# Kernel tuning notes

Measured on AMD Instinct MI355X. Metric: run time of the kernel, lower is better.

## Reference

```python
import jax, jax.numpy as jnp
import numpy as np
from jax import lax

T_LEN, BATCH, IN_DIM, HID = 1024, 64, 256, 256


def setup_inputs() -> dict:
    key = jax.random.key(0)
    k1, k2, k3, k4 = jax.random.split(key, 4)
    x = jax.random.normal(k1, (T_LEN, BATCH, IN_DIM), dtype=jnp.float32)
    m = jax.random.normal(k2, (T_LEN, BATCH, HID), dtype=jnp.float32)
    h0 = jnp.zeros((BATCH, HID), dtype=jnp.float32)
    c0 = jnp.zeros((BATCH, HID), dtype=jnp.float32)
    # 5 gates: input, forget, cell, output, reinstatement
    scale = 1.0 / np.sqrt(HID)
    W_ih = jax.random.normal(k3, (5 * HID, IN_DIM), dtype=jnp.float32) * scale
    W_hh = jax.random.normal(k4, (5 * HID, HID), dtype=jnp.float32) * scale
    b = jnp.zeros((5 * HID,), dtype=jnp.float32)
    return {"x": x, "m": m, "h0": h0, "c0": c0, "W_ih": W_ih, "W_hh": W_hh, "b": b}


def reference(x, m, h0, c0, W_ih, W_hh, b):
    """Episodic LSTM: sequential scan over time (batch_first=False, forward direction).

    x: [T, B, I], m: [T, B, H] (retrieved episodic cell states per step).
    Returns (sequence [T, B, H], h_T [B, H], c_T [B, H]).
    """
    # Precompute input projections for all timesteps in one GEMM: [T, B, 5H]
    x_proj = jnp.einsum("tbi,gi->tbg", x, W_ih) + b

    def step(carry, inp):
        h, c = carry
        xp_t, m_t = inp
        gates = xp_t + h @ W_hh.T  # [B, 5H]
        i, f, g, o, r = jnp.split(gates, 5, axis=-1)
        c = (jax.nn.sigmoid(f) * c
             + jax.nn.sigmoid(i) * jnp.tanh(g)
             + jax.nn.sigmoid(r) * m_t)
        h = jax.nn.sigmoid(o) * jnp.tanh(c)
        return (h, c), h

    (hT, cT), seq = lax.scan(step, (h0, c0), (x_proj, m))
    return seq, hT, cT
```

## Files before the change

kernel.cpp:

```cpp
#include <hip/hip_runtime.h>
#include <stdint.h>
#include <stddef.h>

#define T_LEN 1024
#define BATCH 64
#define KDIM  256
#define HID   256
#define NGATE 5
#define GROWS (NGATE * HID)
#define NGT   (GROWS / 16)
#define NSWG  4

typedef __attribute__((ext_vector_type(8))) short s16x8;
typedef __attribute__((ext_vector_type(4))) float f32x4;
typedef __attribute__((ext_vector_type(4))) int   i32x4;
typedef __attribute__((ext_vector_type(2))) unsigned int u32x2;

static __device__ __forceinline__ uint16_t f2bf(float f) {
  uint32_t u = __float_as_uint(f);
  return (uint16_t)((u + 0x7fffu + ((u >> 16) & 1u)) >> 16);
}
static __device__ __forceinline__ float bf2f(uint16_t b) {
  return __uint_as_float(((uint32_t)b) << 16);
}
static __device__ __forceinline__ s16x8 cvt8(const float* __restrict__ p) {
  float4 a = *reinterpret_cast<const float4*>(p);
  float4 b = *reinterpret_cast<const float4*>(p + 4);
  union { s16x8 v; uint16_t u[8]; } r;
  r.u[0] = f2bf(a.x); r.u[1] = f2bf(a.y); r.u[2] = f2bf(a.z); r.u[3] = f2bf(a.w);
  r.u[4] = f2bf(b.x); r.u[5] = f2bf(b.y); r.u[6] = f2bf(b.z); r.u[7] = f2bf(b.w);
  return r.v;
}
static __device__ __forceinline__ float sigm(float x)   { return 1.f / (1.f + __expf(-x)); }
static __device__ __forceinline__ float tanh_f(float x) { return 1.f - 2.f / (__expf(2.f * x) + 1.f); }
static __device__ __forceinline__ int swz(int row, int col) {
  return ((((col >> 4) ^ (row & 15)) << 4) | (col & 15));
}

__global__ void setup_kernel(const float* __restrict__ Wih, const float* __restrict__ c0,
                             uint16_t* __restrict__ wihb, float* __restrict__ cbuf) {
  int i = blockIdx.x * 256 + threadIdx.x;
  if (i < GROWS * KDIM) wihb[i] = f2bf(Wih[i]);
  if (i < BATCH * HID) cbuf[i] = c0[i];
}

__global__ void wquant_kernel(const float* __restrict__ Whh,
                              int8_t* __restrict__ wq, float* __restrict__ wsc) {
  int row = blockIdx.x * 256 + threadIdx.x;
  if (row >= GROWS) return;
  const float* wr = Whh + (size_t)row * KDIM;
  float mx = 1e-30f;
  for (int k = 0; k < KDIM; ++k) mx = fmaxf(mx, fabsf(wr[k]));
  wsc[row] = mx / 127.f;
  const float inv = 127.f / mx;
  int8_t* q = wq + (size_t)row * KDIM;
  for (int k = 0; k < KDIM; ++k) q[k] = (int8_t)__float2int_rn(wr[k] * inv);
}

__global__ __launch_bounds__(256, 2)
void xproj_kernel(const float* __restrict__ x, const uint16_t* __restrict__ wihb,
                  const float* __restrict__ bias, uint16_t* __restrict__ xp, int t0) {
  const int w = threadIdx.x >> 6, lane = threadIdx.x & 63;
  const int r16 = lane & 15, ke = (lane >> 4) * 8;
  const int tA = t0 + (int)blockIdx.x * 2;

  s16x8 A[2][8];
#pragma unroll
  for (int tt = 0; tt < 2; ++tt) {
    const float* ap = x + ((size_t)(tA + tt) * BATCH + w * 16 + r16) * KDIM + ke;
#pragma unroll
    for (int ks = 0; ks < 8; ++ks) A[tt][ks] = cvt8(ap + ks * 32);
  }
  for (int gt = 0; gt < NGT; ++gt) {
    const uint16_t* bp = wihb + (size_t)(gt * 16 + r16) * KDIM + ke;
    s16x8 B[8];
#pragma unroll
    for (int ks = 0; ks < 8; ++ks) B[ks] = *reinterpret_cast<const s16x8*>(bp + ks * 32);
    const float bv = bias[gt * 16 + r16];
#pragma unroll
    for (int tt = 0; tt < 2; ++tt) {
      f32x4 acc = {};
#pragma unroll
      for (int ks = 0; ks < 8; ++ks)
        acc = __builtin_amdgcn_mfma_f32_16x16x32_bf16(A[tt][ks], B[ks], acc, 0, 0, 0);
      const int lt = (int)blockIdx.x * 2 + tt;
      uint32_t w0 = (uint32_t)f2bf(acc[0] + bv) | ((uint32_t)f2bf(acc[1] + bv) << 16);
      uint32_t w1 = (uint32_t)f2bf(acc[2] + bv) | ((uint32_t)f2bf(acc[3] + bv) << 16);
      u32x2 pk = {w0, w1};
      u32x2* dst = (u32x2*)((uint32_t*)(xp + ((size_t)(lt * 4 + w) * NGT + gt) * 256) + lane * 2);
      __builtin_nontemporal_store(pk, dst);
    }
  }
}

__global__ __launch_bounds__(1024, 4)
void scan_kernel(const float* __restrict__ mIn, const int8_t* __restrict__ wq,
                 const float* __restrict__ wsc, const uint16_t* __restrict__ xp,
                 const float* __restrict__ h_src, float* __restrict__ cbuf,
                 float* __restrict__ seq, float* __restrict__ hT, float* __restrict__ cT,
                 int s0, int s1) {
  struct SW {
    int8_t w[16][2][4][1024];
    int8_t hq[2][16][256];
  };
  __shared__ SW sl;
  const int wg = blockIdx.x;
  const int v = threadIdx.x >> 6;
  const int lane = threadIdx.x & 63;
  const int r16 = lane & 15, g4 = lane >> 4;
  const int bj0 = g4 * 4;
  const int brow = wg * 16;
  const int col = v * 16 + r16;

  i32x4 Wf[3][4];
  float sc[NGATE];
#pragma unroll
  for (int g = 0; g < NGATE; ++g) {
    const int grow = g * 256 + col;
    if (g < 3) {
      const int8_t* wp = wq + (size_t)grow * KDIM + g4 * 16;
#pragma unroll
      for (int ks = 0; ks < 4; ++ks)
        Wf[g][ks] = *reinterpret_cast<const i32x4*>(wp + ks * 64);
    }
    sc[g] = wsc[grow] * (1.f / 127.f);
  }
#pragma unroll
  for (int gl = 0; gl < 2; ++gl) {
    const int grow = (3 + gl) * 256 + col;
    const int8_t* wp = wq + (size_t)grow * KDIM + g4 * 16;
#pragma unroll
    for (int ks = 0; ks < 4; ++ks)
      *reinterpret_cast<i32x4*>(&sl.w[v][gl][ks][lane * 16]) =
          *reinterpret_cast<const i32x4*>(wp + ks * 64);
  }

  float c[4];
#pragma unroll
  for (int j = 0; j < 4; ++j)
    c[j] = cbuf[(size_t)(brow + bj0 + j) * HID + col];

  {
    const int p0 = s0 & 1;
#pragma unroll
    for (int e = 0; e < 4; ++e) {
      int t = (int)threadIdx.x * 4 + e;
      int row = t >> 8, cc = t & 255;
      float hv = h_src[(size_t)(brow + row) * HID + cc];
      int q = __float2int_rn(fminf(fmaxf(hv * 127.f, -127.f), 127.f));
      sl.hq[p0][row][swz(row, cc)] = (int8_t)q;
    }
  }
  __syncthreads();

  const uint16_t* xpb = xp + ((size_t)wg * NGT + v) * 256 + lane * 4;
  const float*    mb  = mIn + ((size_t)s0 * BATCH + brow + bj0) * HID + col;
  float*          sqb = seq + ((size_t)s0 * BATCH + brow + bj0) * HID + col;

  u32x2 xpf[NGATE];
  float mv[4];
#pragma unroll
  for (int g = 0; g < NGATE; ++g)
    xpf[g] = *reinterpret_cast<const u32x2*>(xpb + g * 16 * 256);
#pragma unroll
  for (int j = 0; j < 4; ++j) mv[j] = mb[j * HID];

  for (int s = s0; s < s1; ++s) {
    const int p = s & 1;

    i32x4 acc[NGATE] = {};
    __builtin_amdgcn_s_setprio(1);
#pragma unroll
    for (int ks = 0; ks < 4; ++ks) {
      i32x4 A = *reinterpret_cast<const i32x4*>(&sl.hq[p][r16][swz(r16, (g4 + 4 * ks) * 16)]);
      acc[0] = __builtin_amdgcn_mfma_i32_16x16x64_i8(A, Wf[0][ks], acc[0], 0, 0, 0);
      acc[1] = __builtin_amdgcn_mfma_i32_16x16x64_i8(A, Wf[1][ks], acc[1], 0, 0, 0);
      acc[2] = __builtin_amdgcn_mfma_i32_16x16x64_i8(A, Wf[2][ks], acc[2], 0, 0, 0);
      i32x4 b0 = *reinterpret_cast<const i32x4*>(&sl.w[v][0][ks][lane * 16]);
      acc[3] = __builtin_amdgcn_mfma_i32_16x16x64_i8(A, b0, acc[3], 0, 0, 0);
      i32x4 b1 = *reinterpret_cast<const i32x4*>(&sl.w[v][1][ks][lane * 16]);
      acc[4] = __builtin_amdgcn_mfma_i32_16x16x64_i8(A, b1, acc[4], 0, 0, 0);
    }
    __builtin_amdgcn_s_setprio(0);

    float hnew[4];
#pragma unroll
    for (int j = 0; j < 4; ++j) {
#define XPV(g) bf2f((uint16_t)((j & 1) ? (xpf[g][j >> 1] >> 16) : (xpf[g][j >> 1] & 0xffff)))
      const float gi = (float)acc[0][j] * sc[0] + XPV(0);
      const float gf = (float)acc[1][j] * sc[1] + XPV(1);
      const float gg = (float)acc[2][j] * sc[2] + XPV(2);
      const float go = (float)acc[3][j] * sc[3] + XPV(3);
      const float gr = (float)acc[4][j] * sc[4] + XPV(4);
#undef XPV
      const float cn = sigm(gf) * c[j] + sigm(gi) * tanh_f(gg) + sigm(gr) * mv[j];
      c[j] = cn;
      hnew[j] = sigm(go) * tanh_f(cn);
    }

    const uint16_t* xpb_n = xpb + 4 * NGT * 256;
    const float*    mb_n  = (s + 1 < s1) ? mb + BATCH * HID : mb;
#pragma unroll
    for (int g = 0; g < NGATE; ++g)
      xpf[g] = *reinterpret_cast<const u32x2*>(xpb_n + g * 16 * 256);
#pragma unroll
    for (int j = 0; j < 4; ++j) mv[j] = mb_n[j * HID];
    xpb = xpb_n; mb = mb_n;

#pragma unroll
    for (int j = 0; j < 4; ++j) {
      __builtin_nontemporal_store(hnew[j], sqb + j * HID);
      int q = __float2int_rn(hnew[j] * 127.f);
      sl.hq[p ^ 1][bj0 + j][swz(bj0 + j, col)] = (int8_t)q;
    }
    if (s == T_LEN - 1) {
#pragma unroll
      for (int j = 0; j < 4; ++j) {
        hT[(size_t)(brow + bj0 + j) * HID + col] = hnew[j];
        cT[(size_t)(brow + bj0 + j) * HID + col] = c[j];
      }
    }
    sqb += BATCH * HID;

    __builtin_amdgcn_sched_barrier(0);
    asm volatile("s_waitcnt lgkmcnt(0)" ::: "memory");
    __builtin_amdgcn_s_barrier();
    __builtin_amdgcn_sched_barrier(0);
  }

#pragma unroll
  for (int j = 0; j < 4; ++j)
    cbuf[(size_t)(brow + bj0 + j) * HID + col] = c[j];
}

extern "C" void kernel_launch(void* const* d_in, const int* in_sizes, int n_in,
                              void* d_out, int out_size, void* d_ws, size_t ws_size,
                              hipStream_t stream) {
  (void)in_sizes; (void)n_in; (void)out_size;
  const float* x    = (const float*)d_in[0];
  const float* mIn  = (const float*)d_in[1];
  const float* h0   = (const float*)d_in[2];
  const float* c0   = (const float*)d_in[3];
  const float* Wih  = (const float*)d_in[4];
  const float* Whh  = (const float*)d_in[5];
  const float* bias = (const float*)d_in[6];
  float* out = (float*)d_out;
  float* seq = out;
  float* hT  = out + (size_t)T_LEN * BATCH * HID;
  float* cT  = hT + (size_t)BATCH * HID;

  const size_t fixed = (size_t)GROWS * KDIM * 2 + (size_t)GROWS * KDIM
                     + (size_t)GROWS * 4 + (size_t)BATCH * HID * 4 + 4096;
  int tchunk = T_LEN;
  while (tchunk > 2 && (size_t)tchunk * BATCH * GROWS * 2 + fixed > ws_size) tchunk >>= 1;

  char* p = (char*)d_ws;
  uint16_t* xp   = (uint16_t*)p;  p += (size_t)tchunk * BATCH * GROWS * 2;
  uint16_t* wihb = (uint16_t*)p;  p += (size_t)GROWS * KDIM * 2;
  int8_t*   wq   = (int8_t*)p;    p += (size_t)GROWS * KDIM;
  float*    wsc  = (float*)p;     p += (size_t)GROWS * 4;
  float*    cbuf = (float*)p;

  setup_kernel<<<dim3((GROWS * KDIM + 255) / 256), dim3(256), 0, stream>>>(
      Wih, c0, wihb, cbuf);
  wquant_kernel<<<dim3((GROWS + 255) / 256), dim3(256), 0, stream>>>(Whh, wq, wsc);
  for (int s0 = 0; s0 < T_LEN; s0 += tchunk) {
    xproj_kernel<<<dim3(tchunk / 2), dim3(256), 0, stream>>>(x, wihb, bias, xp, s0);
    const float* h_src = (s0 == 0) ? h0 : (seq + (size_t)(s0 - 1) * BATCH * HID);
    scan_kernel<<<dim3(NSWG), dim3(1024), 0, stream>>>(
        mIn, wq, wsc, xp, h_src, cbuf, seq, hT, cT, s0, s0 + tchunk);
  }
}
```

Measured before the change: 4.004 ms.

## Hold all recurrent weights in AGPRs, fold log2e into weights, unroll scan by two

All five int8 W_hh gate slices now stay in registers, fed to inline-asm MFMAs as AGPR operands, so the two gates that used LDS no longer reload it every step. log2(e) factors are folded into W_ih, the bias and the per-row scales so the activations can use raw v_exp_f32 and v_rcp_f32. The time loop is unrolled by two with separate prefetch buffers for xp and m, which removes the parity math. The trade-offs are higher register pressure and reliance on inline asm, which limits compiler scheduling. The loop also assumes s1-s0 is even and hard-codes parity 0 as the start, which could break for odd chunk boundaries.

Measured after the change: 6.730 ms. 68.1% more time.

```diff
diff --git a/kernel.cpp b/kernel.cpp
--- a/kernel.cpp
+++ b/kernel.cpp
@@ -11,6 +11,9 @@
 #define NGT   (GROWS / 16)
 #define NSWG  4
 
+#define L2E  1.442695041f
+#define L2E2 2.885390082f
+
 typedef __attribute__((ext_vector_type(8))) short s16x8;
 typedef __attribute__((ext_vector_type(4))) float f32x4;
 typedef __attribute__((ext_vector_type(4))) int   i32x4;
@@ -31,16 +34,38 @@
   r.u[4] = f2bf(b.x); r.u[5] = f2bf(b.y); r.u[6] = f2bf(b.z); r.u[7] = f2bf(b.w);
   return r.v;
 }
-static __device__ __forceinline__ float sigm(float x)   { return 1.f / (1.f + __expf(-x)); }
-static __device__ __forceinline__ float tanh_f(float x) { return 1.f - 2.f / (__expf(2.f * x) + 1.f); }
+static __device__ __forceinline__ float rcp_hw(float x) {
+  float r; asm("v_rcp_f32 %0, %1" : "=v"(r) : "v"(x)); return r;
+}
+static __device__ __forceinline__ float exp2_hw(float x) {
+  float r; asm("v_exp_f32 %0, %1" : "=v"(r) : "v"(x)); return r;
+}
+static __device__ __forceinline__ float exp2_neg(float x) {
+  float r; asm("v_exp_f32 %0, -%1" : "=v"(r) : "v"(x)); return r;
+}
+static __device__ __forceinline__ float sigm2(float xs) {
+  return rcp_hw(1.f + exp2_neg(xs));
+}
+static __device__ __forceinline__ float tanh2(float xs) {
+  return __builtin_fmaf(-2.f, rcp_hw(1.f + exp2_hw(xs)), 1.f);
+}
 static __device__ __forceinline__ int swz(int row, int col) {
   return ((((col >> 4) ^ (row & 15)) << 4) | (col & 15));
 }
+
+#define MFMA_A(acc, A, W) \
+  asm("v_mfma_i32_16x16x64_i8 %0, %1, %2, %0" : "+v"(acc) : "v"(A), "a"(W))
+#define MFMA_I(acc, A, W, Z) \
+  asm("v_mfma_i32_16x16x64_i8 %0, %1, %2, %3" : "=&v"(acc) : "v"(A), "a"(W), "v"(Z))
 
 __global__ void setup_kernel(const float* __restrict__ Wih, const float* __restrict__ c0,
                              uint16_t* __restrict__ wihb, float* __restrict__ cbuf) {
   int i = blockIdx.x * 256 + threadIdx.x;
-  if (i < GROWS * KDIM) wihb[i] = f2bf(Wih[i]);
+  if (i < GROWS * KDIM) {
+    int gate = (i >> 8) >> 8;
+    float kg = (gate == 2) ? L2E2 : L2E;
+    wihb[i] = f2bf(Wih[i] * kg);
+  }
   if (i < BATCH * HID) cbuf[i] = c0[i];
 }
 
@@ -76,7 +101,8 @@
     s16x8 B[8];
 #pragma unroll
     for (int ks = 0; ks < 8; ++ks) B[ks] = *reinterpret_cast<const s16x8*>(bp + ks * 32);
-    const float bv = bias[gt * 16 + r16];
+    const float kg = ((gt >> 4) == 2) ? L2E2 : L2E;
+    const float bv = bias[gt * 16 + r16] * kg;
 #pragma unroll
     for (int tt = 0; tt < 2; ++tt) {
       f32x4 acc = {};
@@ -99,11 +125,7 @@
                  const float* __restrict__ h_src, float* __restrict__ cbuf,
                  float* __restrict__ seq, float* __restrict__ hT, float* __restrict__ cT,
                  int s0, int s1) {
-  struct SW {
-    int8_t w[16][2][4][1024];
-    int8_t hq[2][16][256];
-  };
-  __shared__ SW sl;
+  __shared__ int8_t hq[2][16][256];
   const int wg = blockIdx.x;
   const int v = threadIdx.x >> 6;
   const int lane = threadIdx.x & 63;
@@ -112,27 +134,16 @@
   const int brow = wg * 16;
   const int col = v * 16 + r16;
 
-  i32x4 Wf[3][4];
+  i32x4 Wf[NGATE][4];
   float sc[NGATE];
 #pragma unroll
   for (int g = 0; g < NGATE; ++g) {
-    const int grow = g * 256 + col;
-    if (g < 3) {
-      const int8_t* wp = wq + (size_t)grow * KDIM + g4 * 16;
-#pragma unroll
-      for (int ks = 0; ks < 4; ++ks)
-        Wf[g][ks] = *reinterpret_cast<const i32x4*>(wp + ks * 64);
-    }
-    sc[g] = wsc[grow] * (1.f / 127.f);
-  }
-#pragma unroll
-  for (int gl = 0; gl < 2; ++gl) {
-    const int grow = (3 + gl) * 256 + col;
-    const int8_t* wp = wq + (size_t)grow * KDIM + g4 * 16;
+    const float kg = (g == 2) ? L2E2 : L2E;
+    sc[g] = wsc[g * 256 + col] * (kg / 127.f);
+    const int8_t* wp = wq + (size_t)(g * 256 + col) * KDIM + g4 * 16;
 #pragma unroll
     for (int ks = 0; ks < 4; ++ks)
-      *reinterpret_cast<i32x4*>(&sl.w[v][gl][ks][lane * 16]) =
-          *reinterpret_cast<const i32x4*>(wp + ks * 64);
+      Wf[g][ks] = *reinterpret_cast<const i32x4*>(wp + ks * 64);
   }
 
   float c[4];
@@ -140,46 +151,61 @@
   for (int j = 0; j < 4; ++j)
     c[j] = cbuf[(size_t)(brow + bj0 + j) * HID + col];
 
-  {
-    const int p0 = s0 & 1;
-#pragma unroll
-    for (int e = 0; e < 4; ++e) {
-      int t = (int)threadIdx.x * 4 + e;
-      int row = t >> 8, cc = t & 255;
-      float hv = h_src[(size_t)(brow + row) * HID + cc];
-      int q = __float2int_rn(fminf(fmaxf(hv * 127.f, -127.f), 127.f));
-      sl.hq[p0][row][swz(row, cc)] = (int8_t)q;
-    }
+#pragma unroll
+  for (int e = 0; e < 4; ++e) {
+    int t = (int)threadIdx.x * 4 + e;
+    int row = t >> 8, cc = t & 255;
+    float hv = h_src[(size_t)(brow + row) * HID + cc];
+    int q = __float2int_rn(fminf(fmaxf(hv * 127.f, -127.f), 127.f));
+    hq[0][row][swz(row, cc)] = (int8_t)q;
   }
   __syncthreads();
 
-  const uint16_t* xpb = xp + ((size_t)wg * NGT + v) * 256 + lane * 4;
-  const float*    mb  = mIn + ((size_t)s0 * BATCH + brow + bj0) * HID + col;
-  float*          sqb = seq + ((size_t)s0 * BATCH + brow + bj0) * HID + col;
-
-  u32x2 xpf[NGATE];
-  float mv[4];
-#pragma unroll
-  for (int g = 0; g < NGATE; ++g)
-    xpf[g] = *reinterpret_cast<const u32x2*>(xpb + g * 16 * 256);
-#pragma unroll
-  for (int j = 0; j < 4; ++j) mv[j] = mb[j * HID];
-
-  for (int s = s0; s < s1; ++s) {
-    const int p = s & 1;
-
-    i32x4 acc[NGATE] = {};
+  int aoff[4], woff[4];
+#pragma unroll
+  for (int ks = 0; ks < 4; ++ks) aoff[ks] = r16 * 256 + swz(r16, (g4 + 4 * ks) * 16);
+#pragma unroll
+  for (int j = 0; j < 4; ++j) woff[j] = (bj0 + j) * 256 + swz(bj0 + j, col);
+  int8_t* const hq0 = &hq[0][0][0];
+
+  const i32x4 zero4 = {0, 0, 0, 0};
+  const int XPS = 4 * NGT * 256;
+
+  const uint16_t* xpbA = xp + ((size_t)wg * NGT + v) * 256 + lane * 4;
+  const uint16_t* xpbB = xpbA + XPS;
+  const float* mbA = mIn + ((size_t)s0 * BATCH + brow + bj0) * HID + col;
+  const float* mbB = mbA + BATCH * HID;
+  float* sqb = seq + ((size_t)s0 * BATCH + brow + bj0) * HID + col;
+
+  u32x2 xpfA[NGATE], xpfB[NGATE];
+  float mvA[4], mvB[4];
+#pragma unroll
+  for (int g = 0; g < NGATE; ++g) {
+    xpfA[g] = *reinterpret_cast<const u32x2*>(xpbA + g * 4096);
+    xpfB[g] = *reinterpret_cast<const u32x2*>(xpbB + g * 4096);
+  }
+#pragma unroll
+  for (int j = 0; j < 4; ++j) { mvA[j] = mbA[j * HID]; mvB[j] = mbB[j * HID]; }
+
+  auto step = [&](int ss, int par, u32x2 (&xpf)[NGATE], float (&mv)[4],
+                  const uint16_t*& xpb, const float*& mb) {
+    const int8_t* hr = hq0 + par * 4096;
+    int8_t*       hw = hq0 + (par ^ 1) * 4096;
+
+    i32x4 a0, a1, a2, a3, a4;
     __builtin_amdgcn_s_setprio(1);
-#pragma unroll
-    for (int ks = 0; ks < 4; ++ks) {
-      i32x4 A = *reinterpret_cast<const i32x4*>(&sl.hq[p][r16][swz(r16, (g4 + 4 * ks) * 16)]);
-      acc[0] = __builtin_amdgcn_mfma_i32_16x16x64_i8(A, Wf[0][ks], acc[0], 0, 0, 0);
-      acc[1] = __builtin_amdgcn_mfma_i32_16x16x64_i8(A, Wf[1][ks], acc[1], 0, 0, 0);
-      acc[2] = __builtin_amdgcn_mfma_i32_16x16x64_i8(A, Wf[2][ks], acc[2], 0, 0, 0);
-      i32x4 b0 = *reinterpret_cast<const i32x4*>(&sl.w[v][0][ks][lane * 16]);
-      acc[3] = __builtin_amdgcn_mfma_i32_16x16x64_i8(A, b0, acc[3], 0, 0, 0);
-      i32x4 b1 = *reinterpret_cast<const i32x4*>(&sl.w[v][1][ks][lane * 16]);
-      acc[4] = __builtin_amdgcn_mfma_i32_16x16x64_i8(A, b1, acc[4], 0, 0, 0);
+    {
+      i32x4 A = *reinterpret_cast<const i32x4*>(hr + aoff[0]);
+      MFMA_I(a0, A, Wf[0][0], zero4); MFMA_I(a1, A, Wf[1][0], zero4);
+      MFMA_I(a2, A, Wf[2][0], zero4); MFMA_I(a3, A, Wf[3][0], zero4);
+      MFMA_I(a4, A, Wf[4][0], zero4);
+    }
+#pragma unroll
+    for (int ks = 1; ks < 4; ++ks) {
+      i32x4 A = *reinterpret_cast<const i32x4*>(hr + aoff[ks]);
+      MFMA_A(a0, A, Wf[0][ks]); MFMA_A(a1, A, Wf[1][ks]);
+      MFMA_A(a2, A, Wf[2][ks]); MFMA_A(a3, A, Wf[3][ks]);
+      MFMA_A(a4, A, Wf[4][ks]);
     }
     __builtin_amdgcn_s_setprio(0);
 
@@ -187,33 +213,31 @@
 #pragma unroll
     for (int j = 0; j < 4; ++j) {
 #define XPV(g) bf2f((uint16_t)((j & 1) ? (xpf[g][j >> 1] >> 16) : (xpf[g][j >> 1] & 0xffff)))
-      const float gi = (float)acc[0][j] * sc[0] + XPV(0);
-      const float gf = (float)acc[1][j] * sc[1] + XPV(1);
-      const float gg = (float)acc[2][j] * sc[2] + XPV(2);
-      const float go = (float)acc[3][j] * sc[3] + XPV(3);
-      const float gr = (float)acc[4][j] * sc[4] + XPV(4);
+      const float gi = __builtin_fmaf((float)a0[j], sc[0], XPV(0));
+      const float gf = __builtin_fmaf((float)a1[j], sc[1], XPV(1));
+      const float gg = __builtin_fmaf((float)a2[j], sc[2], XPV(2));
+      const float go = __builtin_fmaf((float)a3[j], sc[3], XPV(3));
+      const float gr = __builtin_fmaf((float)a4[j], sc[4], XPV(4));
 #undef XPV
-      const float cn = sigm(gf) * c[j] + sigm(gi) * tanh_f(gg) + sigm(gr) * mv[j];
+      const float cn = sigm2(gf) * c[j] + sigm2(gi) * tanh2(gg) + sigm2(gr) * mv[j];
       c[j] = cn;
-      hnew[j] = sigm(go) * tanh_f(cn);
-    }
-
-    const uint16_t* xpb_n = xpb + 4 * NGT * 256;
-    const float*    mb_n  = (s + 1 < s1) ? mb + BATCH * HID : mb;
+      hnew[j] = sigm2(go) * tanh2(cn * L2E2);
+    }
+
+    xpb += 2 * XPS;
+    mb = (ss + 2 < T_LEN) ? mb + 2 * BATCH * HID : mb;
 #pragma unroll
     for (int g = 0; g < NGATE; ++g)
-      xpf[g] = *reinterpret_cast<const u32x2*>(xpb_n + g * 16 * 256);
-#pragma unroll
-    for (int j = 0; j < 4; ++j) mv[j] = mb_n[j * HID];
-    xpb = xpb_n; mb = mb_n;
+      xpf[g] = *reinterpret_cast<const u32x2*>(xpb + g * 4096);
+#pragma unroll
+    for (int j = 0; j < 4; ++j) mv[j] = mb[j * HID];
 
 #pragma unroll
     for (int j = 0; j < 4; ++j) {
       __builtin_nontemporal_store(hnew[j], sqb + j * HID);
-      int q = __float2int_rn(hnew[j] * 127.f);
-      sl.hq[p ^ 1][bj0 + j][swz(bj0 + j, col)] = (int8_t)q;
-    }
-    if (s == T_LEN - 1) {
+      hw[woff[j]] = (int8_t)__float2int_rn(hnew[j] * 127.f);
+    }
+    if (ss == T_LEN - 1) {
 #pragma unroll
       for (int j = 0; j < 4; ++j) {
         hT[(size_t)(brow + bj0 + j) * HID + col] = hnew[j];
@@ -226,6 +250,11 @@
     asm volatile("s_waitcnt lgkmcnt(0)" ::: "memory");
     __builtin_amdgcn_s_barrier();
     __builtin_amdgcn_sched_barrier(0);
+  };
+
+  for (int s = s0; s < s1; s += 2) {
+    step(s,     0, xpfA, mvA, xpbA, mbA);
+    step(s + 1, 1, xpfB, mvB, xpbB, mbB);
   }
 
 #pragma unroll
```
